# Kernel tuning notes

Measured on AMD Instinct MI355X. Metric: run time of the kernel, lower is better.

Reference implementation:

```python
import jax, jax.numpy as jnp
import numpy as np

STRIDE = 10
NUM_POS = 16
THRESHOLD = 0.5
TEMPERATURE = 0.5
EPS = 1e-8


def _l2norm(x, axis=-1):
    return x / (jnp.linalg.norm(x, axis=axis, keepdims=True) + EPS)


def setup_inputs() -> dict:
    key = jax.random.key(0)
    k1, k2, k3, k4 = jax.random.split(key, 4)
    B, D, K, T, L = 4096, 1024, 131072, 50, 2
    x_q = jax.random.normal(k1, (B, D), dtype=jnp.float32)
    x_label = jax.random.randint(k2, (B, T, L), 0, 2, dtype=jnp.int32)
    queue_features = jax.random.normal(k3, (K, D), dtype=jnp.float32)
    queue_labels = jax.random.randint(k4, (K, T, L), 0, 2, dtype=jnp.int32)
    return {"x_q": x_q, "x_label": x_label,
            "queue_features": queue_features, "queue_labels": queue_labels}


def reference(x_q, x_label, queue_features, queue_labels):
    # Normalize anchor and queue features (as in forward()).
    q = _l2norm(x_q)                      # [B, D]
    k = _l2norm(queue_features)           # [K, D]

    # Deterministic variant of the stride-10 queue scan (start index fixed to 0).
    ks = k[::STRIDE]                      # [Ks, D]
    ql = queue_labels[::STRIDE].astype(jnp.float32)   # [Ks, T, L]
    al = x_label.astype(jnp.float32)                  # [B, T, L]

    # Per-timestep cosine similarity of labels, abs, then mean over timesteps.
    aln = _l2norm(al)                     # [B, T, L]
    qln = _l2norm(ql)                     # [Ks, T, L]
    lab_sim = jnp.mean(jnp.abs(jnp.einsum('btl,ktl->bkt', aln, qln)), axis=-1)  # [B, Ks]

    # Positive mask with early-stop emulation: take the FIRST num_pos_samples
    # entries (in scan order) whose label similarity >= threshold.
    mask = lab_sim >= THRESHOLD                         # [B, Ks]
    rank = jnp.cumsum(mask.astype(jnp.int32), axis=1) - 1
    valid = mask & (rank < NUM_POS)                     # [B, Ks]
    count = jnp.minimum(jnp.sum(mask, axis=1), NUM_POS) # [B]

    # Feature cosine similarities (q, ks are unit norm -> dot product).
    sims = jnp.einsum('bd,kd->bk', q, ks) / TEMPERATURE  # [B, Ks]
    loss_elem = -jax.nn.log_sigmoid(sims)                # [B, Ks]

    per_anchor = jnp.sum(loss_elem * valid.astype(loss_elem.dtype), axis=1)
    per_anchor = jnp.where(count > 0,
                           per_anchor / jnp.maximum(count, 1).astype(loss_elem.dtype),
                           0.0)
    return jnp.mean(per_anchor)
```

## Files before the change

### kernel.cpp

```cpp
#include <hip/hip_runtime.h>
#include <math.h>

#define BB 4096
#define DD 1024
#define TT 50
#define NKS 13108
#define NPOS 16

__global__ __launch_bounds__(256) void label_codes(const int* __restrict__ labels,
                                                   unsigned long long* __restrict__ omask,
                                                   int nrows, int row_mult) {
    int w    = (blockIdx.x * blockDim.x + threadIdx.x) >> 6;
    int lane = threadIdx.x & 63;
    if (w >= nrows) return;
    const int2* p = (const int2*)(labels + (size_t)w * row_mult);
    int l0 = 0, l1 = 0;
    if (lane < TT) { int2 ll = p[lane]; l0 = ll.x; l1 = ll.y; }
    bool a = (lane < TT);
    unsigned long long p0 = __ballot(a && l0 && !l1);
    unsigned long long p1 = __ballot(a && l1 && !l0);
    unsigned long long dd = __ballot(a && l0 && l1);
    if (lane == 0) {
        omask[(size_t)w*3 + 0] = p0;
        omask[(size_t)w*3 + 1] = p1;
        omask[(size_t)w*3 + 2] = dd;
    }
}

__global__ __launch_bounds__(256) void scan_mask(const unsigned long long* __restrict__ bmask,
                                                 const unsigned long long* __restrict__ kmask,
                                                 int* __restrict__ list,
                                                 int* __restrict__ cnt) {
    int b   = blockIdx.x;
    int tid = threadIdx.x;
    int lane = tid & 63, wid = tid >> 6;

    unsigned long long pA0 = bmask[(size_t)b*3 + 0];
    unsigned long long pA1 = bmask[(size_t)b*3 + 1];
    unsigned long long dA  = bmask[(size_t)b*3 + 2];
    unsigned long long sA  = pA0 | pA1;

    const float v = 1.0f / (sqrtf(2.0f) + 1e-8f);
    const float s = v*v + v*v;

    __shared__ int wcnt[4];
    unsigned long long lmask = (1ull << lane) - 1ull;

    int found = 0;
    for (int base = 0; base < NKS; base += 256) {
        int kk = base + tid;
        bool m = false;
        if (kk < NKS) {
            unsigned long long pK0 = kmask[(size_t)kk*3 + 0];
            unsigned long long pK1 = kmask[(size_t)kk*3 + 1];
            unsigned long long dK  = kmask[(size_t)kk*3 + 2];
            unsigned long long sK  = pK0 | pK1;
            unsigned long long mss = (pA0 & pK0) | (pA1 & pK1);
            unsigned long long mdd = dA & dK;
            unsigned long long mix = (dA & sK) | (sA & dK);
            float sum = (float)__popcll(mss) + (float)__popcll(mdd)*s + (float)__popcll(mix)*v;
            m = (sum >= 25.0f);
        }
        unsigned long long bal = __ballot(m);
        if (lane == 0) wcnt[wid] = __popcll(bal);
        __syncthreads();
        int w0 = wcnt[0], w1 = wcnt[1], w2 = wcnt[2], w3 = wcnt[3];
        int woff = (wid > 0 ? w0 : 0) + (wid > 1 ? w1 : 0) + (wid > 2 ? w2 : 0);
        if (m) {
            int pos = found + woff + __popcll(bal & lmask);
            if (pos < NPOS) list[b*NPOS + pos] = kk;
        }
        found += w0 + w1 + w2 + w3;
        __syncthreads();
        if (found >= NPOS) break;
    }
    if (tid == 0) cnt[b] = found < NPOS ? found : NPOS;
}

__device__ inline float2 block_reduce2(float a, float b, float* lds) {
    for (int o = 32; o > 0; o >>= 1) {
        a += __shfl_down(a, o);
        b += __shfl_down(b, o);
    }
    int lane = threadIdx.x & 63, wid = threadIdx.x >> 6;
    if (lane == 0) { lds[wid*2] = a; lds[wid*2 + 1] = b; }
    __syncthreads();
    float2 r;
    r.x = lds[0] + lds[2] + lds[4] + lds[6];
    r.y = lds[1] + lds[3] + lds[5] + lds[7];
    __syncthreads();
    return r;
}

__global__ __launch_bounds__(256) void loss_kernel(const float* __restrict__ x_q,
                                                   const float* __restrict__ qf,
                                                   const int* __restrict__ list,
                                                   const int* __restrict__ cnt,
                                                   float* __restrict__ per_b) {
    int b   = blockIdx.x;
    int tid = threadIdx.x;
    __shared__ float red[8];

    const float4* xqv = (const float4*)(x_q + (size_t)b * DD);
    float4 xq = xqv[tid];
    float nn = xq.x*xq.x + xq.y*xq.y + xq.z*xq.z + xq.w*xq.w;
    float2 nrm = block_reduce2(nn, 0.0f, red);
    float nq = sqrtf(nrm.x) + 1e-8f;

    int count = cnt[b];
    float per_anchor = 0.0f;
    for (int j = 0; j < count; ++j) {
        int kk = list[b*NPOS + j];
        const float4* rv = (const float4*)(qf + (size_t)kk * 10 * DD);
        float4 r = rv[tid];
        float dotp = xq.x*r.x + xq.y*r.y + xq.z*r.z + xq.w*r.w;
        float nk   = r.x*r.x + r.y*r.y + r.z*r.z + r.w*r.w;
        float2 rr = block_reduce2(dotp, nk, red);
        if (tid == 0) {
            float denom = nq * (sqrtf(rr.y) + 1e-8f);
            float sims = (rr.x / denom) * 2.0f;
            float z = -sims;
            per_anchor += fmaxf(z, 0.0f) + log1pf(expf(-fabsf(z)));
        }
    }
    if (tid == 0) {
        per_b[b] = (count > 0) ? per_anchor / (float)count : 0.0f;
    }
}

__global__ __launch_bounds__(256) void final_reduce(const float* __restrict__ per_b,
                                                    float* __restrict__ out) {
    int tid = threadIdx.x;
    float s = 0.0f;
    for (int i = tid; i < BB; i += 256) s += per_b[i];
    for (int o = 32; o > 0; o >>= 1) s += __shfl_down(s, o);
    __shared__ float red[4];
    int lane = tid & 63, wid = tid >> 6;
    if (lane == 0) red[wid] = s;
    __syncthreads();
    if (tid == 0) out[0] = (red[0] + red[1] + red[2] + red[3]) * (1.0f / (float)BB);
}

extern "C" void kernel_launch(void* const* d_in, const int* in_sizes, int n_in,
                              void* d_out, int out_size, void* d_ws, size_t ws_size,
                              hipStream_t stream) {
    const float* x_q            = (const float*)d_in[0];
    const int*   x_label        = (const int*)d_in[1];
    const float* queue_features = (const float*)d_in[2];
    const int*   queue_labels   = (const int*)d_in[3];
    float* out = (float*)d_out;

    unsigned long long* bmask = (unsigned long long*)d_ws;
    unsigned long long* kmask = bmask + (size_t)BB * 3;
    int* list  = (int*)(kmask + (size_t)NKS * 3);
    int* cnt   = list + (size_t)BB * NPOS;
    float* per_b = (float*)(cnt + BB);

    label_codes<<<BB*64/256, 256, 0, stream>>>(x_label, bmask, BB, TT*2);
    label_codes<<<(NKS*64 + 255)/256, 256, 0, stream>>>(queue_labels, kmask, NKS, TT*2*10);

    scan_mask<<<BB, 256, 0, stream>>>(bmask, kmask, list, cnt);
    loss_kernel<<<BB, 256, 0, stream>>>(x_q, queue_features, list, cnt, per_b);
    final_reduce<<<1, 256, 0, stream>>>(per_b, out);
}
```

Baseline: 710.5 us.

## Fuse label-code launches and merge scan with loss using wave-level reductions

The two label_codes launches become one launch covering both anchor and queue rows. The mask scan and the loss computation are fused into one kernel, so the positive list lives in shared memory instead of global memory. The scan loop drops one barrier by double-buffering the per-wave counts. The loss phase gives each wave a whole queue row, reduced with a wave-level shuffle, so the per-row block barriers go away. This cuts launch count, global round trips and synchronisation, but concentrates the feature gathers into fewer waves per row.

```diff
diff --git a/kernel.cpp b/kernel.cpp
--- a/kernel.cpp
+++ b/kernel.cpp
@@ -6,125 +6,121 @@
 #define TT 50
 #define NKS 13108
 #define NPOS 16
+#define NW_TOTAL (BB + NKS)
 
-__global__ __launch_bounds__(256) void label_codes(const int* __restrict__ labels,
-                                                   unsigned long long* __restrict__ omask,
-                                                   int nrows, int row_mult) {
+__global__ __launch_bounds__(256) void label_codes_all(const int* __restrict__ xl,
+                                                       const int* __restrict__ ql,
+                                                       unsigned long long* __restrict__ bmask,
+                                                       unsigned long long* __restrict__ kmask) {
     int w    = (blockIdx.x * blockDim.x + threadIdx.x) >> 6;
     int lane = threadIdx.x & 63;
-    if (w >= nrows) return;
-    const int2* p = (const int2*)(labels + (size_t)w * row_mult);
+    if (w >= NW_TOTAL) return;
+    const int2* p;
+    unsigned long long* o;
+    if (w < BB) {
+        p = (const int2*)(xl + (size_t)w * (TT * 2));
+        o = bmask + (size_t)w * 3;
+    } else {
+        int kk = w - BB;
+        p = (const int2*)(ql + (size_t)kk * (TT * 2 * 10));
+        o = kmask + (size_t)kk * 3;
+    }
     int l0 = 0, l1 = 0;
     if (lane < TT) { int2 ll = p[lane]; l0 = ll.x; l1 = ll.y; }
     bool a = (lane < TT);
     unsigned long long p0 = __ballot(a && l0 && !l1);
     unsigned long long p1 = __ballot(a && l1 && !l0);
     unsigned long long dd = __ballot(a && l0 && l1);
-    if (lane == 0) {
-        omask[(size_t)w*3 + 0] = p0;
-        omask[(size_t)w*3 + 1] = p1;
-        omask[(size_t)w*3 + 2] = dd;
-    }
+    if (lane == 0) { o[0] = p0; o[1] = p1; o[2] = dd; }
 }
 
-__global__ __launch_bounds__(256) void scan_mask(const unsigned long long* __restrict__ bmask,
+__device__ inline float d4(float4 a, float4 b) {
+    return a.x * b.x + a.y * b.y + a.z * b.z + a.w * b.w;
+}
+
+__global__ __launch_bounds__(256) void scan_loss(const unsigned long long* __restrict__ bmask,
                                                  const unsigned long long* __restrict__ kmask,
-                                                 int* __restrict__ list,
-                                                 int* __restrict__ cnt) {
-    int b   = blockIdx.x;
-    int tid = threadIdx.x;
+                                                 const float* __restrict__ x_q,
+                                                 const float* __restrict__ qf,
+                                                 float* __restrict__ per_b) {
+    int b    = blockIdx.x;
+    int tid  = threadIdx.x;
     int lane = tid & 63, wid = tid >> 6;
 
-    unsigned long long pA0 = bmask[(size_t)b*3 + 0];
-    unsigned long long pA1 = bmask[(size_t)b*3 + 1];
-    unsigned long long dA  = bmask[(size_t)b*3 + 2];
+    unsigned long long pA0 = bmask[(size_t)b * 3 + 0];
+    unsigned long long pA1 = bmask[(size_t)b * 3 + 1];
+    unsigned long long dA  = bmask[(size_t)b * 3 + 2];
     unsigned long long sA  = pA0 | pA1;
 
     const float v = 1.0f / (sqrtf(2.0f) + 1e-8f);
-    const float s = v*v + v*v;
+    const float s = v * v + v * v;
 
-    __shared__ int wcnt[4];
+    __shared__ int   wcnt[2][4];
+    __shared__ int   slist[NPOS];
+    __shared__ float red[4];
     unsigned long long lmask = (1ull << lane) - 1ull;
 
     int found = 0;
+    int ph = 0;
     for (int base = 0; base < NKS; base += 256) {
         int kk = base + tid;
         bool m = false;
         if (kk < NKS) {
-            unsigned long long pK0 = kmask[(size_t)kk*3 + 0];
-            unsigned long long pK1 = kmask[(size_t)kk*3 + 1];
-            unsigned long long dK  = kmask[(size_t)kk*3 + 2];
+            unsigned long long pK0 = kmask[(size_t)kk * 3 + 0];
+            unsigned long long pK1 = kmask[(size_t)kk * 3 + 1];
+            unsigned long long dK  = kmask[(size_t)kk * 3 + 2];
             unsigned long long sK  = pK0 | pK1;
             unsigned long long mss = (pA0 & pK0) | (pA1 & pK1);
             unsigned long long mdd = dA & dK;
             unsigned long long mix = (dA & sK) | (sA & dK);
-            float sum = (float)__popcll(mss) + (float)__popcll(mdd)*s + (float)__popcll(mix)*v;
+            float sum = (float)__popcll(mss) + (float)__popcll(mdd) * s + (float)__popcll(mix) * v;
             m = (sum >= 25.0f);
         }
         unsigned long long bal = __ballot(m);
-        if (lane == 0) wcnt[wid] = __popcll(bal);
+        if (lane == 0) wcnt[ph][wid] = __popcll(bal);
         __syncthreads();
-        int w0 = wcnt[0], w1 = wcnt[1], w2 = wcnt[2], w3 = wcnt[3];
+        int w0 = wcnt[ph][0], w1 = wcnt[ph][1], w2 = wcnt[ph][2], w3 = wcnt[ph][3];
         int woff = (wid > 0 ? w0 : 0) + (wid > 1 ? w1 : 0) + (wid > 2 ? w2 : 0);
         if (m) {
             int pos = found + woff + __popcll(bal & lmask);
-            if (pos < NPOS) list[b*NPOS + pos] = kk;
+            if (pos < NPOS) slist[pos] = kk;
         }
         found += w0 + w1 + w2 + w3;
-        __syncthreads();
+        ph ^= 1;
         if (found >= NPOS) break;
     }
-    if (tid == 0) cnt[b] = found < NPOS ? found : NPOS;
-}
+    int count = found < NPOS ? found : NPOS;
+    __syncthreads();
 
-__device__ inline float2 block_reduce2(float a, float b, float* lds) {
-    for (int o = 32; o > 0; o >>= 1) {
-        a += __shfl_down(a, o);
-        b += __shfl_down(b, o);
-    }
-    int lane = threadIdx.x & 63, wid = threadIdx.x >> 6;
-    if (lane == 0) { lds[wid*2] = a; lds[wid*2 + 1] = b; }
-    __syncthreads();
-    float2 r;
-    r.x = lds[0] + lds[2] + lds[4] + lds[6];
-    r.y = lds[1] + lds[3] + lds[5] + lds[7];
-    __syncthreads();
-    return r;
-}
+    const float4* xr = (const float4*)(x_q + (size_t)b * DD);
+    float4 xq0 = xr[lane], xq1 = xr[lane + 64], xq2 = xr[lane + 128], xq3 = xr[lane + 192];
+    float nn = d4(xq0, xq0) + d4(xq1, xq1) + d4(xq2, xq2) + d4(xq3, xq3);
+    for (int o = 32; o > 0; o >>= 1) nn += __shfl_xor(nn, o);
+    float nq = sqrtf(nn) + 1e-8f;
 
-__global__ __launch_bounds__(256) void loss_kernel(const float* __restrict__ x_q,
-                                                   const float* __restrict__ qf,
-                                                   const int* __restrict__ list,
-                                                   const int* __restrict__ cnt,
-                                                   float* __restrict__ per_b) {
-    int b   = blockIdx.x;
-    int tid = threadIdx.x;
-    __shared__ float red[8];
-
-    const float4* xqv = (const float4*)(x_q + (size_t)b * DD);
-    float4 xq = xqv[tid];
-    float nn = xq.x*xq.x + xq.y*xq.y + xq.z*xq.z + xq.w*xq.w;
-    float2 nrm = block_reduce2(nn, 0.0f, red);
-    float nq = sqrtf(nrm.x) + 1e-8f;
-
-    int count = cnt[b];
-    float per_anchor = 0.0f;
-    for (int j = 0; j < count; ++j) {
-        int kk = list[b*NPOS + j];
+    float part = 0.0f;
+    for (int j = wid; j < count; j += 4) {
+        int kk = slist[j];
         const float4* rv = (const float4*)(qf + (size_t)kk * 10 * DD);
-        float4 r = rv[tid];
-        float dotp = xq.x*r.x + xq.y*r.y + xq.z*r.z + xq.w*r.w;
-        float nk   = r.x*r.x + r.y*r.y + r.z*r.z + r.w*r.w;
-        float2 rr = block_reduce2(dotp, nk, red);
-        if (tid == 0) {
-            float denom = nq * (sqrtf(rr.y) + 1e-8f);
-            float sims = (rr.x / denom) * 2.0f;
+        float4 r0 = rv[lane], r1 = rv[lane + 64], r2 = rv[lane + 128], r3 = rv[lane + 192];
+        float dotp = d4(xq0, r0) + d4(xq1, r1) + d4(xq2, r2) + d4(xq3, r3);
+        float nk   = d4(r0, r0) + d4(r1, r1) + d4(r2, r2) + d4(r3, r3);
+        for (int o = 32; o > 0; o >>= 1) {
+            dotp += __shfl_xor(dotp, o);
+            nk   += __shfl_xor(nk, o);
+        }
+        if (lane == 0) {
+            float denom = nq * (sqrtf(nk) + 1e-8f);
+            float sims = (dotp / denom) * 2.0f;
             float z = -sims;
-            per_anchor += fmaxf(z, 0.0f) + log1pf(expf(-fabsf(z)));
+            part += fmaxf(z, 0.0f) + log1pf(expf(-fabsf(z)));
         }
     }
+    if (lane == 0) red[wid] = part;
+    __syncthreads();
     if (tid == 0) {
-        per_b[b] = (count > 0) ? per_anchor / (float)count : 0.0f;
+        float pa = red[0] + red[1] + red[2] + red[3];
+        per_b[b] = (count > 0) ? pa / (float)count : 0.0f;
     }
 }
 
@@ -152,14 +148,12 @@
 
     unsigned long long* bmask = (unsigned long long*)d_ws;
     unsigned long long* kmask = bmask + (size_t)BB * 3;
-    int* list  = (int*)(kmask + (size_t)NKS * 3);
-    int* cnt   = list + (size_t)BB * NPOS;
-    float* per_b = (float*)(cnt + BB);
+    float* per_b = (float*)(kmask + (size_t)NKS * 3);
 
-    label_codes<<<BB*64/256, 256, 0, stream>>>(x_label, bmask, BB, TT*2);
-    label_codes<<<(NKS*64 + 255)/256, 256, 0, stream>>>(queue_labels, kmask, NKS, TT*2*10);
+    label_codes_all<<<(NW_TOTAL * 64 + 255) / 256, 256, 0, stream>>>(
+        x_label, queue_labels, bmask, kmask);
 
-    scan_mask<<<BB, 256, 0, stream>>>(bmask, kmask, list, cnt);
-    loss_kernel<<<BB, 256, 0, stream>>>(x_q, queue_features, list, cnt, per_b);
+    scan_loss<<<BB, 256, 0, stream>>>(bmask, kmask, x_q, queue_features, per_b);
+
     final_reduce<<<1, 256, 0, stream>>>(per_b, out);
 }
```

Measured after the change: 677.6 us. -4.6%, faster.
